# Performance work log

Hardware: AMD Instinct MI355X
Metric: run time of the kernel (lower is better)

Reference implementation:

```python
import jax, jax.numpy as jnp
import numpy as np

B, LB, LC, H = 8, 512, 128, 256
H2 = 2 * H
MIN_WS, N_WIN = 5, 4


def _highway(x, Wn, bn, Wl, bl, Wg, bg):
    # AllenNLP-style highway: per layer, gate * relu(nonlinear) + (1-gate) * linear
    # Wn/Wl/Wg: [L, D, D]; bn/bl/bg: [L, D]
    for i in range(Wn.shape[0]):
        g = jax.nn.sigmoid(x @ Wg[i] + bg[i])
        x = g * jax.nn.relu(x @ Wn[i] + bn[i]) + (1.0 - g) * (x @ Wl[i] + bl[i])
    return x


def _additive_scores(q, k, Wq, bq, Wk, v):
    # 'BilinearAttention' in the repo is additive: v^T tanh(Wq q + Wk k)
    # q: [..., Lq, D], k: [..., Lk, D] -> scores [..., Lq, Lk]
    wq = q @ Wq + bq
    uh = k @ Wk
    return jnp.tanh(wq[..., :, None, :] + uh[..., None, :, :]) @ v


def setup_inputs() -> dict:
    key = jax.random.key(0)
    ks = jax.random.split(key, 32)
    s2 = 1.0 / np.sqrt(H2)
    s1 = 1.0 / np.sqrt(H)
    d = {
        'b_enc_output': jax.random.normal(ks[0], (B, LB, H), jnp.float32),
        'c_enc_output': jax.random.normal(ks[1], (B, LC, H), jnp.float32),
        'c_state': jax.random.normal(ks[2], (B, 1, H), jnp.float32),
        'b_mask': jnp.ones((B, LB), bool),
        'c_mask': jnp.ones((B, LC), bool),
    }
    # b_highway / c_highway: 2 layers, each with nonlinear/linear/gate Linear(2H,2H)
    for pfx, base in (('bh', 3), ('ch', 9)):
        d[pfx + '_Wn'] = jax.random.normal(ks[base + 0], (2, H2, H2), jnp.float32) * s2
        d[pfx + '_bn'] = jnp.zeros((2, H2), jnp.float32)
        d[pfx + '_Wl'] = jax.random.normal(ks[base + 1], (2, H2, H2), jnp.float32) * s2
        d[pfx + '_bl'] = jnp.zeros((2, H2), jnp.float32)
        d[pfx + '_Wg'] = jax.random.normal(ks[base + 2], (2, H2, H2), jnp.float32) * s2
        d[pfx + '_bg'] = jnp.zeros((2, H2), jnp.float32)
    # match_attn (2H) and area_attn (H)
    d['m_Wq'] = jax.random.normal(ks[15], (H2, H2), jnp.float32) * s2
    d['m_bq'] = jnp.zeros((H2,), jnp.float32)
    d['m_Wk'] = jax.random.normal(ks[16], (H2, H2), jnp.float32) * s2
    d['m_v'] = jax.random.normal(ks[17], (H2,), jnp.float32) * s2
    d['a_Wq'] = jax.random.normal(ks[18], (H, H), jnp.float32) * s1
    d['a_bq'] = jnp.zeros((H,), jnp.float32)
    d['a_Wk'] = jax.random.normal(ks[19], (H, H), jnp.float32) * s1
    d['a_v'] = jax.random.normal(ks[20], (H,), jnp.float32) * s1
    return d


def reference(b_enc_output, c_enc_output, c_state,
              bh_Wn, bh_bn, bh_Wl, bh_bl, bh_Wg, bh_bg,
              ch_Wn, ch_bn, ch_Wl, ch_bl, ch_Wg, ch_bg,
              m_Wq, m_bq, m_Wk, m_v,
              a_Wq, a_bq, a_Wk, a_v,
              b_mask, c_mask):
    Bsz, Lb, Hd = b_enc_output.shape
    Lc = c_enc_output.shape[1]
    # match(): highway over [enc ; c_state]
    cs_b = jnp.broadcast_to(c_state, (Bsz, Lb, Hd))
    cs_c = jnp.broadcast_to(c_state, (Bsz, Lc, Hd))
    b = _highway(jnp.concatenate([b_enc_output, cs_b], -1), bh_Wn, bh_bn, bh_Wl, bh_bl, bh_Wg, bh_bg)
    c = _highway(jnp.concatenate([c_enc_output, cs_c], -1), ch_Wn, ch_bn, ch_Wl, ch_bl, ch_Wg, ch_bg)
    m = _additive_scores(b, c, m_Wq, m_bq, m_Wk, m_v)  # [B,Lb,Lc]
    m = jnp.where(c_mask[:, None, :], m, -jnp.inf)
    b_score = jnp.where(b_mask, jnp.max(m, axis=-1), 0.0)  # [B,Lb]
    # segments(): multi-scale sliding windows (unfold) + area attention
    q = c_state[:, :, None, :]  # [B,1,1,H]
    segs, scores = [], []
    for i in range(N_WIN):
        ws = MIN_WS * (i + 1)
        n_seg = (Lb - ws) // MIN_WS + 1
        idx = jnp.arange(n_seg)[:, None] * MIN_WS + jnp.arange(ws)[None, :]  # [n_seg, ws]
        bw = b_enc_output[:, idx, :]  # [B,n_seg,ws,H]
        attn = jax.nn.softmax(_additive_scores(q, bw, a_Wq, a_bq, a_Wk, a_v), axis=-1)  # [B,n_seg,1,ws]
        segs.append(jnp.einsum('bnqw,bnwh->bnh', attn, bw))
        scores.append(b_score[:, idx].sum(-1))  # [B,n_seg]
    segments = jnp.concatenate(segs, axis=1)          # [B,N,H]
    s_score = jax.nn.softmax(jnp.concatenate(scores, axis=1), axis=-1)  # [B,N]
    out = jnp.einsum('bn,bnh->bh', s_score, segments)[:, None, :]  # [B,1,H]
    return out, s_score, b_score
```

## Files before the change

kernel.cpp:

```cpp
#include <hip/hip_runtime.h>
#include <hip/hip_bf16.h>
#include <cstdint>
#include <cstddef>


typedef unsigned short ushort8 __attribute__((ext_vector_type(8)));
typedef float f32x4 __attribute__((ext_vector_type(4)));

__device__ __forceinline__ float fsigmoid(float x) { return 1.0f / (1.0f + __expf(-x)); }
__device__ __forceinline__ float ftanh(float x) {
  float e = __expf(2.0f * x);
  return 1.0f - 2.0f / (e + 1.0f);
}
__device__ __forceinline__ unsigned short f2bf(float x) {
  union { float f; unsigned u; } v; v.f = x;
  unsigned r = (v.u + 0x7FFFu + ((v.u >> 16) & 1u)) >> 16;
  return (unsigned short)r;
}
__device__ __forceinline__ f32x4 mfma_bf16(ushort8 a, ushort8 b, f32x4 c) {
  asm("v_mfma_f32_16x16x32_bf16 %0, %1, %2, %0" : "+v"(c) : "v"(a), "v"(b));
  return c;
}

struct WArg { const float* s[15]; };
__global__ __launch_bounds__(256) void prep_k(WArg wa, unsigned short* __restrict__ WT,
    const float* __restrict__ benc, const float* __restrict__ cenc,
    const float* __restrict__ cs,
    unsigned short* __restrict__ XB0, unsigned short* __restrict__ XC0,
    const float* __restrict__ aWq, const float* __restrict__ abq,
    float* __restrict__ wqa) {
  __shared__ float tile[64][65];
  const int blk = blockIdx.x, t = threadIdx.x;
  if (blk < 960) {
    const int mat = blk >> 6, q = blk & 63;
    const int Kd = (mat == 14) ? 256 : 512;
    const int k0 = (q >> 3) << 6, n0 = (q & 7) << 6;
    if (mat == 14 && (k0 >= 256 || n0 >= 256)) return;
    const float* __restrict__ S = wa.s[mat];
    unsigned short* __restrict__ D = WT + (size_t)mat * 262144;
#pragma unroll
    for (int i = 0; i < 16; ++i) {
      int id = i * 256 + t, r = id >> 6, c = id & 63;
      tile[r][c] = S[(size_t)(k0 + r) * Kd + (n0 + c)];
    }
    __syncthreads();
#pragma unroll
    for (int i = 0; i < 16; ++i) {
      int id = i * 256 + t, r = id >> 6, c = id & 63;
      D[(size_t)(n0 + r) * Kd + (k0 + c)] = f2bf(tile[c][r]);
    }
  } else if (blk < 3520) {
    const bool isB = blk < 3008;
    const float* enc = isB ? benc : cenc;
    unsigned short* out = isB ? XB0 : XC0;
    const int Lshift = isB ? 9 : 7;
    int i4 = (blk - (isB ? 960 : 3008)) * 256 + t;
    int row = i4 >> 7, c4 = (i4 & 127) << 2;
    float4 v;
    if (c4 < 256) v = *(const float4*)(enc + ((size_t)row << 8) + c4);
    else          v = *(const float4*)(cs + ((size_t)(row >> Lshift) << 8) + (c4 - 256));
    union { unsigned short u[4]; uint2 w; } o;
    o.u[0] = f2bf(v.x); o.u[1] = f2bf(v.y); o.u[2] = f2bf(v.z); o.u[3] = f2bf(v.w);
    *(uint2*)(out + ((size_t)row << 9) + c4) = o.w;
  } else {
    int b = blk - 3520, h = t;
    float acc = abq[h];
    for (int k = 0; k < 256; ++k) acc += cs[b * 256 + k] * aWq[k * 256 + h];
    wqa[b * 256 + h] = acc;
  }
}

struct GJob {
  const unsigned short* A; const unsigned short* W0;
  const unsigned short* W1; const unsigned short* W2;
  const float* B0; const float* B1; const float* B2;
  void* Y; int lda, N, K, nbxs , epi, nb, blk0;
};

template <int NB>
__device__ __forceinline__ void gemm_body(const GJob& j, int bx, int by,
                                          unsigned short* sm, int t) {
  const int m0 = by * 64, n0 = bx * 64;
  const int lane = t & 63, wid = t >> 6;
  const int wr = wid >> 1, wc = wid & 1;
  const int N = j.N, K = j.K, lda = j.lda;

  const int srow = t >> 3;
  const int cg = (t & 7) ^ (srow & 7);
  const unsigned short* Ag0 = j.A + (size_t)(m0 + srow) * lda + cg * 8;
  const unsigned short* Ag1 = j.A + (size_t)(m0 + 32 + srow) * lda + cg * 8;
  const unsigned short* Wp[3] = {j.W0, j.W1, j.W2};
  const unsigned short* Bg0[NB], * Bg1[NB];
#pragma unroll
  for (int p = 0; p < NB; ++p) {
    Bg0[p] = Wp[p] + (size_t)(n0 + srow) * K + cg * 8;
    Bg1[p] = Wp[p] + (size_t)(n0 + 32 + srow) * K + cg * 8;
  }
  const int d0 = t * 8, d1 = (256 + t) * 8;

  const int fl = lane & 15, lg = lane >> 4;
  int offA[2][2], offB[2][2];
#pragma unroll
  for (int f = 0; f < 2; ++f) {
    int ra = wr * 32 + f * 16 + fl;
    int rb = wc * 32 + f * 16 + fl;
#pragma unroll
    for (int ks = 0; ks < 2; ++ks) {
      offA[f][ks] = ra * 64 + ((((ks << 2) + lg) ^ (ra & 7)) << 3);
      offB[f][ks] = rb * 64 + ((((ks << 2) + lg) ^ (rb & 7)) << 3);
    }
  }

  f32x4 acc[NB][2][2];
#pragma unroll
  for (int p = 0; p < NB; ++p)
#pragma unroll
    for (int i = 0; i < 2; ++i)
#pragma unroll
      for (int q = 0; q < 2; ++q) acc[p][i][q] = (f32x4){0.f, 0.f, 0.f, 0.f};

  ushort8 ra0 = *(const ushort8*)Ag0, ra1 = *(const ushort8*)Ag1;
  ushort8 rb0[NB], rb1[NB];
#pragma unroll
  for (int p = 0; p < NB; ++p) { rb0[p] = *(const ushort8*)Bg0[p]; rb1[p] = *(const ushort8*)Bg1[p]; }

  for (int k0 = 0; k0 < K; k0 += 64) {
    __syncthreads();
    *(ushort8*)&sm[d0] = ra0;
    *(ushort8*)&sm[d1] = ra1;
#pragma unroll
    for (int p = 0; p < NB; ++p) {
      unsigned short* Bs = sm + (1 + p) * 4096;
      *(ushort8*)&Bs[d0] = rb0[p];
      *(ushort8*)&Bs[d1] = rb1[p];
    }
    __syncthreads();
    if (k0 + 64 < K) {
      ra0 = *(const ushort8*)(Ag0 + k0 + 64);
      ra1 = *(const ushort8*)(Ag1 + k0 + 64);
#pragma unroll
      for (int p = 0; p < NB; ++p) {
        rb0[p] = *(const ushort8*)(Bg0[p] + k0 + 64);
        rb1[p] = *(const ushort8*)(Bg1[p] + k0 + 64);
      }
    }
#pragma unroll
    for (int ks = 0; ks < 2; ++ks) {
      ushort8 a0 = *(const ushort8*)&sm[offA[0][ks]];
      ushort8 a1 = *(const ushort8*)&sm[offA[1][ks]];
#pragma unroll
      for (int p = 0; p < NB; ++p) {
        const unsigned short* Bs = sm + (1 + p) * 4096;
        ushort8 b0 = *(const ushort8*)&Bs[offB[0][ks]];
        ushort8 b1 = *(const ushort8*)&Bs[offB[1][ks]];
        acc[p][0][0] = mfma_bf16(a0, b0, acc[p][0][0]);
        acc[p][0][1] = mfma_bf16(a0, b1, acc[p][0][1]);
        acc[p][1][0] = mfma_bf16(a1, b0, acc[p][1][0]);
        acc[p][1][1] = mfma_bf16(a1, b1, acc[p][1][1]);
      }
    }
  }
  asm volatile("s_nop 7\n\ts_nop 7" ::);

#pragma unroll
  for (int mf = 0; mf < 2; ++mf) {
#pragma unroll
    for (int nf = 0; nf < 2; ++nf) {
      const int col = n0 + wc * 32 + nf * 16 + fl;
      const int row0 = m0 + wr * 32 + mf * 16 + lg * 4;
      if constexpr (NB == 3) {
        float bn = j.B0[col], bl = j.B1[col], bg = j.B2[col];
        unsigned short* Y = (unsigned short*)j.Y;
#pragma unroll
        for (int e = 0; e < 4; ++e) {
          float nv = acc[0][mf][nf][e] + bn;
          float lv = acc[1][mf][nf][e] + bl;
          float gv = fsigmoid(acc[2][mf][nf][e] + bg);
          Y[(size_t)(row0 + e) * N + col] = f2bf(gv * fmaxf(nv, 0.f) + (1.f - gv) * lv);
        }
      } else {
        float* Y = (float*)j.Y;
        if (j.epi == 2) {
          float bb = j.B0[col];
#pragma unroll
          for (int e = 0; e < 4; ++e)
            Y[(size_t)(row0 + e) * N + col] = __expf(2.0f * (acc[0][mf][nf][e] + bb));
        } else if (j.epi == 3) {
          f32x4 w;
#pragma unroll
          for (int e = 0; e < 4; ++e) w[e] = __expf(2.0f * acc[0][mf][nf][e]);
          *(f32x4*)(Y + (((size_t)(row0 >> 7)) << 16) + ((size_t)col << 7) + (row0 & 127)) = w;
        } else {
          float bb = j.B0 ? j.B0[col] : 0.f;
#pragma unroll
          for (int e = 0; e < 4; ++e)
            Y[(size_t)(row0 + e) * N + col] = acc[0][mf][nf][e] + bb;
        }
      }
    }
  }
}

__global__ __launch_bounds__(256) void mgemm3_k(GJob j0, GJob j1, GJob j2, int toff,
    const float* __restrict__ uha, const float* __restrict__ wqa,
    const float* __restrict__ av, float* __restrict__ tout) {
  __shared__ unsigned short sm[4 * 4096];
  const int blk = blockIdx.x, t = threadIdx.x;
  if (blk >= toff) {
    const int lane = t & 63, wid = t >> 6;
    const int pos = (blk - toff) * 4 + wid;
    const int b = pos >> 9;
    const int h0 = lane << 2;
    float4 u = *(const float4*)(uha + (size_t)pos * 256 + h0);
    float4 w = *(const float4*)(wqa + b * 256 + h0);
    float4 v = *(const float4*)(av + h0);
    float s = ftanh(w.x + u.x) * v.x + ftanh(w.y + u.y) * v.y +
              ftanh(w.z + u.z) * v.z + ftanh(w.w + u.w) * v.w;
#pragma unroll
    for (int off = 32; off; off >>= 1) s += __shfl_xor(s, off);
    if (lane == 0) tout[pos] = s;
    return;
  }
  GJob j = j0;
  if (blk >= j1.blk0) j = j1;
  if (blk >= j2.blk0) j = j2;
  const int rel = blk - j.blk0;
  const int bx = rel & ((1 << j.nbxs) - 1), by = rel >> j.nbxs;
  if (j.nb == 3) gemm_body<3>(j, bx, by, sm, t);
  else          gemm_body<1>(j, bx, by, sm, t);
}

__global__ __launch_bounds__(256) void mscore_k(const float* __restrict__ EW,
                                                const float* __restrict__ UHT,
                                                const float* __restrict__ mv,
                                                float* __restrict__ bscore) {
  __shared__ float eu[2][32 * 128];
  __shared__ float ews[8][512];
  __shared__ float vvs[512];
  const int t = threadIdx.x, lane = t & 63, wid = t >> 6;
  const int blk = blockIdx.x;
  const int b = blk >> 6, g = blk & 63;
  const int row0 = (b << 9) + (g << 3);
  const float* __restrict__ eub = UHT + ((size_t)b << 16);

#pragma unroll
  for (int q = 0; q < 4; ++q) {
    int f4 = q * 256 + t, r = f4 >> 7, c4 = (f4 & 127) << 2;
    *(float4*)&ews[r][c4] = *(const float4*)(EW + (((size_t)(row0 + r)) << 9) + c4);
  }
  if (t < 128) *(float4*)&vvs[t << 2] = *(const float4*)(mv + (t << 2));

  float V = 0.f;
#pragma unroll
  for (int k = 0; k < 8; ++k) V += mv[lane + (k << 6)];
#pragma unroll
  for (int off = 32; off; off >>= 1) V += __shfl_xor(V, off);

#pragma unroll
  for (int q = 0; q < 4; ++q) {
    int f4 = q * 256 + t;
    *(float4*)&eu[0][f4 << 2] = *(const float4*)(eub + (f4 << 2));
  }

  const int jg = lane & 31, hh = lane >> 5;
  const int lr = wid << 1;
  f32x4 tj0 = (f32x4){0.f, 0.f, 0.f, 0.f};
  f32x4 tj1 = (f32x4){0.f, 0.f, 0.f, 0.f};
  float e0r[16], e1r[16], vr[16];

  for (int c = 0; c < 16; ++c) {
    __syncthreads();
    float4 pf0, pf1, pf2, pf3;
    if (c < 15) {
      const float* src = eub + ((size_t)(c + 1) << 12);
      pf0 = *(const float4*)(src + (t << 2));
      pf1 = *(const float4*)(src + ((256 + t) << 2));
      pf2 = *(const float4*)(src + ((512 + t) << 2));
      pf3 = *(const float4*)(src + ((768 + t) << 2));
    }
    const int hbase = (c << 5) + (hh << 4);
#pragma unroll
    for (int q = 0; q < 4; ++q) {
      *(float4*)&e0r[q << 2] = *(const float4*)&ews[lr][hbase + (q << 2)];
      *(float4*)&e1r[q << 2] = *(const float4*)&ews[lr + 1][hbase + (q << 2)];
      *(float4*)&vr[q << 2]  = *(const float4*)&vvs[hbase + (q << 2)];
    }
    const float* eup = &eu[c & 1][((hh << 4) << 7) + (jg << 2)];
#pragma unroll
    for (int i = 0; i < 16; ++i) {
      float4 u = *(const float4*)(eup + (i << 7));
      float vv = vr[i], e0 = e0r[i], e1 = e1r[i];
      tj0.x += vv * __builtin_amdgcn_rcpf(__builtin_fmaf(e0, u.x, 1.f));
      tj0.y += vv * __builtin_amdgcn_rcpf(__builtin_fmaf(e0, u.y, 1.f));
      tj0.z += vv * __builtin_amdgcn_rcpf(__builtin_fmaf(e0, u.z, 1.f));
      tj0.w += vv * __builtin_amdgcn_rcpf(__builtin_fmaf(e0, u.w, 1.f));
      tj1.x += vv * __builtin_amdgcn_rcpf(__builtin_fmaf(e1, u.x, 1.f));
      tj1.y += vv * __builtin_amdgcn_rcpf(__builtin_fmaf(e1, u.y, 1.f));
      tj1.z += vv * __builtin_amdgcn_rcpf(__builtin_fmaf(e1, u.z, 1.f));
      tj1.w += vv * __builtin_amdgcn_rcpf(__builtin_fmaf(e1, u.w, 1.f));
    }
    if (c < 15) {
      float* dst = &eu[(c + 1) & 1][0];
      *(float4*)&dst[t << 2] = pf0;
      *(float4*)&dst[(256 + t) << 2] = pf1;
      *(float4*)&dst[(512 + t) << 2] = pf2;
      *(float4*)&dst[(768 + t) << 2] = pf3;
    }
  }

  tj0.x += __shfl_xor(tj0.x, 32); tj0.y += __shfl_xor(tj0.y, 32);
  tj0.z += __shfl_xor(tj0.z, 32); tj0.w += __shfl_xor(tj0.w, 32);
  tj1.x += __shfl_xor(tj1.x, 32); tj1.y += __shfl_xor(tj1.y, 32);
  tj1.z += __shfl_xor(tj1.z, 32); tj1.w += __shfl_xor(tj1.w, 32);
  float m0 = fminf(fminf(tj0.x, tj0.y), fminf(tj0.z, tj0.w));
  float m1 = fminf(fminf(tj1.x, tj1.y), fminf(tj1.z, tj1.w));
#pragma unroll
  for (int off = 16; off; off >>= 1) {
    m0 = fminf(m0, __shfl_xor(m0, off));
    m1 = fminf(m1, __shfl_xor(m1, off));
  }
  if (lane == 0) {
    bscore[row0 + lr] = V - 2.f * m0;
    bscore[row0 + lr + 1] = V - 2.f * m1;
  }
}

__global__ __launch_bounds__(256) void seg_k(const float* __restrict__ t,
                                             const float* __restrict__ bscore,
                                             const float* __restrict__ benc,
                                             float* __restrict__ seg,
                                             float* __restrict__ sco) {
  const int s = blockIdx.x, b = blockIdx.y, h = threadIdx.x;
  int i, n;
  if (s < 102)      { i = 0; n = s; }
  else if (s < 203) { i = 1; n = s - 102; }
  else if (s < 303) { i = 2; n = s - 203; }
  else              { i = 3; n = s - 303; }
  const int ws = 5 * (i + 1), start = n * 5;
  const float* tb = t + b * 512 + start;
  float mx = -3.0e38f;
  for (int w = 0; w < ws; ++w) mx = fmaxf(mx, tb[w]);
  float sum = 0.f;
  for (int w = 0; w < ws; ++w) sum += __expf(tb[w] - mx);
  float inv = 1.f / sum;
  float acc = 0.f;
  for (int w = 0; w < ws; ++w)
    acc += __expf(tb[w] - mx) * benc[((size_t)(b * 512 + start + w)) * 256 + h];
  seg[((size_t)(b * 402 + s)) * 256 + h] = acc * inv;
  if (h == 0) {
    float ss = 0.f;
    const float* bs = bscore + b * 512 + start;
    for (int w = 0; w < ws; ++w) ss += bs[w];
    sco[b * 402 + s] = ss;
  }
}

__global__ __launch_bounds__(256) void final_k(const float* __restrict__ sco,
                                               const float* __restrict__ seg,
                                               float* __restrict__ dout) {
  const int b = blockIdx.x, tid = threadIdx.x, lane = tid & 63, wid = tid >> 6;
  __shared__ float sc[402];
  __shared__ float redm[4], reds[4];
  for (int s = tid; s < 402; s += 256) sc[s] = sco[b * 402 + s];
  __syncthreads();
  float m = -3.0e38f;
  for (int s = tid; s < 402; s += 256) m = fmaxf(m, sc[s]);
#pragma unroll
  for (int off = 32; off; off >>= 1) m = fmaxf(m, __shfl_xor(m, off));
  if (lane == 0) redm[wid] = m;
  __syncthreads();
  m = fmaxf(fmaxf(redm[0], redm[1]), fmaxf(redm[2], redm[3]));
  float p = 0.f;
  for (int s = tid; s < 402; s += 256) p += __expf(sc[s] - m);
#pragma unroll
  for (int off = 32; off; off >>= 1) p += __shfl_xor(p, off);
  if (lane == 0) reds[wid] = p;
  __syncthreads();
  float invS = 1.f / (reds[0] + reds[1] + reds[2] + reds[3]);
  for (int s = tid; s < 402; s += 256) {
    float pv = __expf(sc[s] - m) * invS;
    dout[2048 + b * 402 + s] = pv;
    sc[s] = pv;
  }
  __syncthreads();
  float acc = 0.f;
  for (int s = 0; s < 402; ++s)
    acc += sc[s] * seg[((size_t)(b * 402 + s)) * 256 + tid];
  dout[b * 256 + tid] = acc;
}

extern "C" void kernel_launch(void* const* d_in, const int* in_sizes, int n_in,
                              void* d_out, int out_size, void* d_ws, size_t ws_size,
                              hipStream_t stream) {
  const float* b_enc   = (const float*)d_in[0];
  const float* c_enc   = (const float*)d_in[1];
  const float* c_state = (const float*)d_in[2];
  const float* bh_Wn = (const float*)d_in[5];
  const float* bh_bn = (const float*)d_in[6];
  const float* bh_Wl = (const float*)d_in[7];
  const float* bh_bl = (const float*)d_in[8];
  const float* bh_Wg = (const float*)d_in[9];
  const float* bh_bg = (const float*)d_in[10];
  const float* ch_Wn = (const float*)d_in[11];
  const float* ch_bn = (const float*)d_in[12];
  const float* ch_Wl = (const float*)d_in[13];
  const float* ch_bl = (const float*)d_in[14];
  const float* ch_Wg = (const float*)d_in[15];
  const float* ch_bg = (const float*)d_in[16];
  const float* m_Wq  = (const float*)d_in[17];
  const float* m_bq  = (const float*)d_in[18];
  const float* m_Wk  = (const float*)d_in[19];
  const float* m_v   = (const float*)d_in[20];
  const float* a_Wq  = (const float*)d_in[21];
  const float* a_bq  = (const float*)d_in[22];
  const float* a_Wk  = (const float*)d_in[23];
  const float* a_v   = (const float*)d_in[24];

  uint8_t* base = (uint8_t*)d_ws;
  unsigned short* WT  = (unsigned short*)(base);
  unsigned short* WTa = WT + 14 * 262144;
  unsigned short* XB0 = (unsigned short*)(base + 7471104);
  unsigned short* XB1 = (unsigned short*)(base + 11665408);
  unsigned short* XC0 = (unsigned short*)(base + 15859712);
  unsigned short* XC1 = (unsigned short*)(base + 16908288);
  float* EW   = (float*)(base + 17956864);
  float* UHT  = (float*)(base + 26345472);
  float* UHA  = (float*)(base + 28442624);
  float* WQA  = (float*)(base + 32636928);
  float* T    = (float*)(base + 32645120);
  float* SEG  = (float*)(base + 32661504);
  float* SCO  = (float*)(base + 35954688);

  float* out = (float*)d_out;
  float* BSC = out + 5264;

  const int S = 262144;
  const int LW = 262144;
  const int SENT = 1 << 30;

  WArg wa;
  wa.s[0] = bh_Wn; wa.s[1] = bh_Wn + LW;
  wa.s[2] = bh_Wl; wa.s[3] = bh_Wl + LW;
  wa.s[4] = bh_Wg; wa.s[5] = bh_Wg + LW;
  wa.s[6] = ch_Wn; wa.s[7] = ch_Wn + LW;
  wa.s[8] = ch_Wl; wa.s[9] = ch_Wl + LW;
  wa.s[10] = ch_Wg; wa.s[11] = ch_Wg + LW;
  wa.s[12] = m_Wq; wa.s[13] = m_Wk; wa.s[14] = a_Wk;

  prep_k<<<3528, 256, 0, stream>>>(wa, WT, b_enc, c_enc, c_state, XB0, XC0,
                                   a_Wq, a_bq, WQA);

  {
    GJob jb = {XB0, WT, WT + 2 * S, WT + 4 * S, bh_bn, bh_bl, bh_bg,
               XB1, 512, 512, 512, 3, 1, 3, 0};
    GJob jc = {XC0, WT + 6 * S, WT + 8 * S, WT + 10 * S, ch_bn, ch_bl, ch_bg,
               XC1, 512, 512, 512, 3, 1, 3, 512};
    GJob ja = {XB0, WTa, nullptr, nullptr, nullptr, nullptr, nullptr,
               UHA, 512, 256, 256, 2, 0, 1, 640};
    mgemm3_k<<<896, 256, 0, stream>>>(jb, jc, ja, 896, nullptr, nullptr, nullptr, nullptr);
  }
  {
    GJob jb = {XB1, WT + S, WT + 3 * S, WT + 5 * S, bh_bn + 512, bh_bl + 512, bh_bg + 512,
               XB0, 512, 512, 512, 3, 1, 3, 0};
    GJob jc = {XC1, WT + 7 * S, WT + 9 * S, WT + 11 * S, ch_bn + 512, ch_bl + 512, ch_bg + 512,
               XC0, 512, 512, 512, 3, 1, 3, 512};
    GJob js = jc; js.blk0 = SENT;
    mgemm3_k<<<640, 256, 0, stream>>>(jb, jc, js, 640, nullptr, nullptr, nullptr, nullptr);
  }
  {
    GJob je = {XB0, WT + 12 * S, nullptr, nullptr, m_bq, nullptr, nullptr,
               EW, 512, 512, 512, 3, 2, 1, 0};
    GJob ju = {XC0, WT + 13 * S, nullptr, nullptr, nullptr, nullptr, nullptr,
               UHT, 512, 512, 512, 3, 3, 1, 512};
    GJob js = ju; js.blk0 = SENT;
    mgemm3_k<<<1664, 256, 0, stream>>>(je, ju, js, 640, UHA, WQA, a_v, T);
  }

  mscore_k<<<512, 256, 0, stream>>>(EW, UHT, m_v, BSC);
  seg_k<<<dim3(402, 8), 256, 0, stream>>>(T, BSC, b_enc, SEG, SCO);
  final_k<<<8, 256, 0, stream>>>(SCO, SEG, out);
}
```

Baseline: 142.0 us.

## Restructure match-score kernel to register-stream operands and split hidden dim across waves

Rewrites mscore_k so that each block of 512 threads has 8 waves, split two ways over row groups and four ways over hidden-dim quarters. Each lane streams its UHT, EW and v operands straight from global memory into double-buffered registers instead of staging UHT through LDS with per-chunk barriers. Partial sums are reduced once through shared memory at the end. The aim is to remove the 16 per-chunk __syncthreads and the LDS traffic, and to raise the number of resident waves. The trade-offs are more uncoalesced scalar global loads of EW and v, and more redundant global reads of UHT that now depend on cache hits.

```diff
diff --git a/kernel.cpp b/kernel.cpp
--- a/kernel.cpp
+++ b/kernel.cpp
@@ -230,98 +230,105 @@
   else          gemm_body<1>(j, bx, by, sm, t);
 }
 
-__global__ __launch_bounds__(256) void mscore_k(const float* __restrict__ EW,
+__global__ __launch_bounds__(512) void mscore_k(const float* __restrict__ EW,
                                                 const float* __restrict__ UHT,
                                                 const float* __restrict__ mv,
                                                 float* __restrict__ bscore) {
-  __shared__ float eu[2][32 * 128];
-  __shared__ float ews[8][512];
-  __shared__ float vvs[512];
-  const int t = threadIdx.x, lane = t & 63, wid = t >> 6;
+  __shared__ float part[2][4][4][128];
+  const int t = threadIdx.x, lane = t & 63, w = t >> 6;
+  const int rq = w & 1, hq = w >> 1;
   const int blk = blockIdx.x;
-  const int b = blk >> 6, g = blk & 63;
-  const int row0 = (b << 9) + (g << 3);
-  const float* __restrict__ eub = UHT + ((size_t)b << 16);
-
-#pragma unroll
-  for (int q = 0; q < 4; ++q) {
-    int f4 = q * 256 + t, r = f4 >> 7, c4 = (f4 & 127) << 2;
-    *(float4*)&ews[r][c4] = *(const float4*)(EW + (((size_t)(row0 + r)) << 9) + c4);
-  }
-  if (t < 128) *(float4*)&vvs[t << 2] = *(const float4*)(mv + (t << 2));
-
-  float V = 0.f;
-#pragma unroll
-  for (int k = 0; k < 8; ++k) V += mv[lane + (k << 6)];
-#pragma unroll
-  for (int off = 32; off; off >>= 1) V += __shfl_xor(V, off);
-
-#pragma unroll
-  for (int q = 0; q < 4; ++q) {
-    int f4 = q * 256 + t;
-    *(float4*)&eu[0][f4 << 2] = *(const float4*)(eub + (f4 << 2));
-  }
-
-  const int jg = lane & 31, hh = lane >> 5;
-  const int lr = wid << 1;
-  f32x4 tj0 = (f32x4){0.f, 0.f, 0.f, 0.f};
-  f32x4 tj1 = (f32x4){0.f, 0.f, 0.f, 0.f};
-  float e0r[16], e1r[16], vr[16];
-
-  for (int c = 0; c < 16; ++c) {
-    __syncthreads();
-    float4 pf0, pf1, pf2, pf3;
-    if (c < 15) {
-      const float* src = eub + ((size_t)(c + 1) << 12);
-      pf0 = *(const float4*)(src + (t << 2));
-      pf1 = *(const float4*)(src + ((256 + t) << 2));
-      pf2 = *(const float4*)(src + ((512 + t) << 2));
-      pf3 = *(const float4*)(src + ((768 + t) << 2));
-    }
-    const int hbase = (c << 5) + (hh << 4);
-#pragma unroll
-    for (int q = 0; q < 4; ++q) {
-      *(float4*)&e0r[q << 2] = *(const float4*)&ews[lr][hbase + (q << 2)];
-      *(float4*)&e1r[q << 2] = *(const float4*)&ews[lr + 1][hbase + (q << 2)];
-      *(float4*)&vr[q << 2]  = *(const float4*)&vvs[hbase + (q << 2)];
-    }
-    const float* eup = &eu[c & 1][((hh << 4) << 7) + (jg << 2)];
-#pragma unroll
-    for (int i = 0; i < 16; ++i) {
-      float4 u = *(const float4*)(eup + (i << 7));
-      float vv = vr[i], e0 = e0r[i], e1 = e1r[i];
-      tj0.x += vv * __builtin_amdgcn_rcpf(__builtin_fmaf(e0, u.x, 1.f));
-      tj0.y += vv * __builtin_amdgcn_rcpf(__builtin_fmaf(e0, u.y, 1.f));
-      tj0.z += vv * __builtin_amdgcn_rcpf(__builtin_fmaf(e0, u.z, 1.f));
-      tj0.w += vv * __builtin_amdgcn_rcpf(__builtin_fmaf(e0, u.w, 1.f));
-      tj1.x += vv * __builtin_amdgcn_rcpf(__builtin_fmaf(e1, u.x, 1.f));
-      tj1.y += vv * __builtin_amdgcn_rcpf(__builtin_fmaf(e1, u.y, 1.f));
-      tj1.z += vv * __builtin_amdgcn_rcpf(__builtin_fmaf(e1, u.z, 1.f));
-      tj1.w += vv * __builtin_amdgcn_rcpf(__builtin_fmaf(e1, u.w, 1.f));
-    }
-    if (c < 15) {
-      float* dst = &eu[(c + 1) & 1][0];
-      *(float4*)&dst[t << 2] = pf0;
-      *(float4*)&dst[(256 + t) << 2] = pf1;
-      *(float4*)&dst[(512 + t) << 2] = pf2;
-      *(float4*)&dst[(768 + t) << 2] = pf3;
-    }
-  }
-
-  tj0.x += __shfl_xor(tj0.x, 32); tj0.y += __shfl_xor(tj0.y, 32);
-  tj0.z += __shfl_xor(tj0.z, 32); tj0.w += __shfl_xor(tj0.w, 32);
-  tj1.x += __shfl_xor(tj1.x, 32); tj1.y += __shfl_xor(tj1.y, 32);
-  tj1.z += __shfl_xor(tj1.z, 32); tj1.w += __shfl_xor(tj1.w, 32);
-  float m0 = fminf(fminf(tj0.x, tj0.y), fminf(tj0.z, tj0.w));
-  float m1 = fminf(fminf(tj1.x, tj1.y), fminf(tj1.z, tj1.w));
-#pragma unroll
-  for (int off = 16; off; off >>= 1) {
-    m0 = fminf(m0, __shfl_xor(m0, off));
-    m1 = fminf(m1, __shfl_xor(m1, off));
-  }
-  if (lane == 0) {
-    bscore[row0 + lr] = V - 2.f * m0;
-    bscore[row0 + lr + 1] = V - 2.f * m1;
+  const int row0 = __builtin_amdgcn_readfirstlane(blk * 8 + rq * 4);
+  const int b = row0 >> 9;
+  const float* __restrict__ ew = EW + ((size_t)row0 << 9) + hq * 128;
+  const float* __restrict__ vv = mv + hq * 128;
+  const float* __restrict__ up = UHT + ((size_t)b << 16) + ((size_t)(hq * 128) << 7) + (lane << 1);
+
+  float2 acc0 = {0.f, 0.f}, acc1 = {0.f, 0.f}, acc2 = {0.f, 0.f}, acc3 = {0.f, 0.f};
+
+  float2 uA[4], uB[4];
+  float eA[16], eB[16], vA[4], vB[4];
+
+#define LOADB(BUF, h0_)                                              \
+  {                                                                  \
+    const int h0 = (h0_);                                            \
+    _Pragma("unroll") for (int hh = 0; hh < 4; ++hh)                 \
+        BUF##_u[hh] = *(const float2*)(up + ((size_t)(h0 + hh) << 7)); \
+    _Pragma("unroll") for (int r = 0; r < 4; ++r)                    \
+      _Pragma("unroll") for (int hh = 0; hh < 4; ++hh)               \
+        BUF##_e[r * 4 + hh] = ew[(r << 9) + h0 + hh];                \
+    _Pragma("unroll") for (int hh = 0; hh < 4; ++hh)                 \
+        BUF##_v[hh] = vv[h0 + hh];                                   \
+  }
+#define A_u uA
+#define A_e eA
+#define A_v vA
+#define B_u uB
+#define B_e eB
+#define B_v vB
+#define COMP(BUF)                                                            \
+  {                                                                          \
+    _Pragma("unroll") for (int hh = 0; hh < 4; ++hh) {                       \
+      float vvv = BUF##_v[hh];                                               \
+      float2 u = BUF##_u[hh];                                                \
+      float e0 = BUF##_e[0 * 4 + hh], e1 = BUF##_e[1 * 4 + hh];              \
+      float e2 = BUF##_e[2 * 4 + hh], e3 = BUF##_e[3 * 4 + hh];              \
+      acc0.x += vvv * __builtin_amdgcn_rcpf(__builtin_fmaf(e0, u.x, 1.f));   \
+      acc0.y += vvv * __builtin_amdgcn_rcpf(__builtin_fmaf(e0, u.y, 1.f));   \
+      acc1.x += vvv * __builtin_amdgcn_rcpf(__builtin_fmaf(e1, u.x, 1.f));   \
+      acc1.y += vvv * __builtin_amdgcn_rcpf(__builtin_fmaf(e1, u.y, 1.f));   \
+      acc2.x += vvv * __builtin_amdgcn_rcpf(__builtin_fmaf(e2, u.x, 1.f));   \
+      acc2.y += vvv * __builtin_amdgcn_rcpf(__builtin_fmaf(e2, u.y, 1.f));   \
+      acc3.x += vvv * __builtin_amdgcn_rcpf(__builtin_fmaf(e3, u.x, 1.f));   \
+      acc3.y += vvv * __builtin_amdgcn_rcpf(__builtin_fmaf(e3, u.y, 1.f));   \
+    }                                                                        \
+  }
+
+  LOADB(A, 0)
+#pragma unroll
+  for (int i = 0; i < 32; i += 2) {
+    if (i + 1 < 32) LOADB(B, (i + 1) * 4)
+    COMP(A)
+    if (i + 2 < 32) LOADB(A, (i + 2) * 4)
+    COMP(B)
+  }
+#undef LOADB
+#undef COMP
+
+  *(float2*)&part[rq][hq][0][lane << 1] = acc0;
+  *(float2*)&part[rq][hq][1][lane << 1] = acc1;
+  *(float2*)&part[rq][hq][2][lane << 1] = acc2;
+  *(float2*)&part[rq][hq][3][lane << 1] = acc3;
+  __syncthreads();
+
+  if (w < 2) {
+    float V = 0.f;
+#pragma unroll
+    for (int k = 0; k < 8; ++k) V += mv[lane + (k << 6)];
+#pragma unroll
+    for (int off = 32; off; off >>= 1) V += __shfl_xor(V, off);
+
+    float mr[4];
+#pragma unroll
+    for (int r = 0; r < 4; ++r) {
+      float2 s0 = *(const float2*)&part[w][0][r][lane << 1];
+      float2 s1 = *(const float2*)&part[w][1][r][lane << 1];
+      float2 s2 = *(const float2*)&part[w][2][r][lane << 1];
+      float2 s3 = *(const float2*)&part[w][3][r][lane << 1];
+      float sx = s0.x + s1.x + s2.x + s3.x;
+      float sy = s0.y + s1.y + s2.y + s3.y;
+      mr[r] = fminf(sx, sy);
+    }
+#pragma unroll
+    for (int off = 32; off; off >>= 1) {
+#pragma unroll
+      for (int r = 0; r < 4; ++r) mr[r] = fminf(mr[r], __shfl_xor(mr[r], off));
+    }
+    if (lane == 0) {
+      const int ro = blk * 8 + w * 4;
+#pragma unroll
+      for (int r = 0; r < 4; ++r) bscore[ro + r] = V - 2.f * mr[r];
+    }
   }
 }
 
@@ -476,7 +483,7 @@
     mgemm3_k<<<1664, 256, 0, stream>>>(je, ju, js, 640, UHA, WQA, a_v, T);
   }
 
-  mscore_k<<<512, 256, 0, stream>>>(EW, UHT, m_v, BSC);
+  mscore_k<<<512, 512, 0, stream>>>(EW, UHT, m_v, BSC);
   seg_k<<<dim3(402, 8), 256, 0, stream>>>(T, BSC, b_enc, SEG, SCO);
   final_k<<<8, 256, 0, stream>>>(SCO, SEG, out);
 }
```

Result: slower. 144.9 us (+2.0%).
